# Optimization experiments

Hardware: AMD Instinct MI355X
Metric: run time of the kernel (lower is better)

## Reference

```python
import jax, jax.numpy as jnp
import numpy as np

D_MODEL = 2048
N_HEADS = 16
HEAD_DIM = D_MODEL // N_HEADS
BATCH = 2
SEQ = 2048


def rotate_half(x):
    x1, x2 = jnp.split(x, 2, axis=-1)
    return jnp.concatenate((-x2, x1), axis=-1)


def rope_emb(seq_len, head_dim, dtype=jnp.float32):
    inv_freq = 1.0 / (10000.0 ** (jnp.arange(0, head_dim, 2, dtype=jnp.float32) / head_dim))
    t = jnp.arange(seq_len, dtype=jnp.float32)
    freqs = jnp.einsum('i,j->ij', t, inv_freq)            # [S, D/2]
    emb = jnp.concatenate((freqs, freqs), axis=-1)        # [S, D]
    return emb[None, :, None, :].astype(dtype)            # [1, S, 1, D]


def apply_rope(x, emb):
    return x * jnp.cos(emb) + rotate_half(x) * jnp.sin(emb)


def setup_inputs() -> dict:
    key = jax.random.key(0)
    ks = jax.random.split(key, 5)
    s = 1.0 / np.sqrt(D_MODEL)
    return {
        'query': jax.random.normal(ks[0], (BATCH, SEQ, D_MODEL), jnp.float32),
        'Wq': jax.random.normal(ks[1], (D_MODEL, D_MODEL), jnp.float32) * s,
        'Wk': jax.random.normal(ks[2], (D_MODEL, D_MODEL), jnp.float32) * s,
        'Wv': jax.random.normal(ks[3], (D_MODEL, D_MODEL), jnp.float32) * s,
        'Wo': jax.random.normal(ks[4], (D_MODEL, D_MODEL), jnp.float32) * s,
    }


def reference(query, Wq, Wk, Wv, Wo):
    B, S, _ = query.shape
    # QKV projections (nn.Linear: x @ W.T), reshape to [B, S, H, Dh]
    q = (query @ Wq.T).reshape(B, S, N_HEADS, HEAD_DIM)
    k = (query @ Wk.T).reshape(B, S, N_HEADS, HEAD_DIM)
    v = (query @ Wv.T).reshape(B, S, N_HEADS, HEAD_DIM)
    emb = rope_emb(S, HEAD_DIM, q.dtype)
    q = apply_rope(q, emb)
    k = apply_rope(k, emb)
    # causal SDPA
    scale = HEAD_DIM ** -0.5
    scores = jnp.einsum('bqhd,bkhd->bhqk', q, k) * scale  # [B, H, S, S]
    causal = jnp.tril(jnp.ones((S, S), dtype=bool))
    scores = jnp.where(causal, scores, jnp.finfo(scores.dtype).min)
    attn = jax.nn.softmax(scores, axis=-1)
    out = jnp.einsum('bhqk,bkhd->bqhd', attn, v).reshape(B, S, D_MODEL)
    return out @ Wo.T
```

## Files before the change

kernel.cpp:

```cpp
#include <hip/hip_runtime.h>
#include <math.h>

#define BATCH 2
#define SEQ 2048
#define DMODEL 2048
#define NHEADS 16
#define HEADDIM 128
#define MTOT (BATCH * SEQ)
#define QKVLD 6144

typedef __attribute__((ext_vector_type(8))) _Float16 half8;
typedef __attribute__((ext_vector_type(4))) _Float16 half4;
typedef __attribute__((ext_vector_type(4))) float f32x4;

__device__ __forceinline__ void gl_lds16(const void* g, void* l) {
    __builtin_amdgcn_global_load_lds(
        (const __attribute__((address_space(1))) unsigned int*)g,
        (__attribute__((address_space(3))) unsigned int*)l, 16, 0, 0);
}

__global__ __launch_bounds__(256) void f2h_conv(const float* __restrict__ src,
                                                _Float16* __restrict__ dst) {
    size_t i = ((size_t)blockIdx.x * 256 + threadIdx.x) * 8;
    float4 a = *(const float4*)(src + i);
    float4 b = *(const float4*)(src + i + 4);
    union { uint4 u; _Float16 h[8]; } o;
    o.h[0] = (_Float16)a.x; o.h[1] = (_Float16)a.y;
    o.h[2] = (_Float16)a.z; o.h[3] = (_Float16)a.w;
    o.h[4] = (_Float16)b.x; o.h[5] = (_Float16)b.y;
    o.h[6] = (_Float16)b.z; o.h[7] = (_Float16)b.w;
    *(uint4*)(dst + i) = o.u;
}

__global__ __launch_bounds__(256) void f2h3_conv(const float* __restrict__ s0,
                                                 const float* __restrict__ s1,
                                                 const float* __restrict__ s2,
                                                 _Float16* __restrict__ dst) {
    const float* src = (blockIdx.y == 0) ? s0 : (blockIdx.y == 1) ? s1 : s2;
    size_t i = ((size_t)blockIdx.x * 256 + threadIdx.x) * 8;
    float4 a = *(const float4*)(src + i);
    float4 b = *(const float4*)(src + i + 4);
    union { uint4 u; _Float16 h[8]; } o;
    o.h[0] = (_Float16)a.x; o.h[1] = (_Float16)a.y;
    o.h[2] = (_Float16)a.z; o.h[3] = (_Float16)a.w;
    o.h[4] = (_Float16)b.x; o.h[5] = (_Float16)b.y;
    o.h[6] = (_Float16)b.z; o.h[7] = (_Float16)b.w;
    *(uint4*)(dst + (size_t)blockIdx.y * (DMODEL * DMODEL) + i) = o.u;
}

#define SB0  __builtin_amdgcn_sched_barrier(0)
#define BAR  __builtin_amdgcn_s_barrier()
#define VMW4 do { SB0; asm volatile("s_waitcnt vmcnt(4)"); SB0; } while (0)
#define VMW0 do { SB0; asm volatile("s_waitcnt vmcnt(0)"); SB0; } while (0)

template <bool F16OUT>
__global__ __launch_bounds__(512, 2) void gemm8p(const _Float16* __restrict__ A,
                                                 const _Float16* __restrict__ W,
                                                 void* __restrict__ Cout,
                                                 int M, int N, int K) {
    __shared__ __align__(16) _Float16 LAb[2][2][128][64];
    __shared__ __align__(16) _Float16 LBb[2][2][128][64];

    const int tid = threadIdx.x;
    const int lane = tid & 63;
    const int wave = tid >> 6;
    const int quad = lane >> 4;
    const int lcol = lane & 15;
    const int wr = wave >> 2;
    const int wc = wave & 3;
    const int m0 = blockIdx.y * 256;
    const int n0 = blockIdx.x * 256;

    const int srow = tid >> 3;
    const int sc8p = tid & 7;
    const int sc8l = sc8p ^ (srow & 7);

#define STA(BUF, HALF, KT)                                                     \
    do {                                                                       \
        _Pragma("unroll") for (int j = 0; j < 2; j++)                          \
            gl_lds16(A + (size_t)(m0 + (HALF)*128 + j*64 + srow) * K +         \
                         (KT)*64 + sc8l*8,                                     \
                     &LAb[BUF][HALF][j*64 + srow][sc8p*8]);                    \
    } while (0)
#define STB(BUF, HALF, KT)                                                     \
    do {                                                                       \
        _Pragma("unroll") for (int j = 0; j < 2; j++)                          \
            gl_lds16(W + (size_t)(n0 + (HALF)*128 + j*64 + srow) * K +         \
                         (KT)*64 + sc8l*8,                                     \
                     &LBb[BUF][HALF][j*64 + srow][sc8p*8]);                    \
    } while (0)

    auto rdA = [&](int buf, int mf, int ks) -> half8 {
        int R = mf * 16 + lcol;
        return *(const half8*)&LAb[buf][wr][R]
                [(ks * 32 + quad * 8) ^ ((lcol & 7) << 3)];
    };
    auto rdB = [&](int buf, int nf, int ks) -> half8 {
        int R = (wc & 1) * 64 + nf * 16 + lcol;
        return *(const half8*)&LBb[buf][wc >> 1][R]
                [(ks * 32 + quad * 8) ^ ((lcol & 7) << 3)];
    };

    f32x4 acc[8][4];
#pragma unroll
    for (int i = 0; i < 8; i++)
#pragma unroll
        for (int j = 0; j < 4; j++) acc[i][j] = (f32x4){0.f, 0.f, 0.f, 0.f};

#define KTILE4(BUF, S1, S2, S3, S4, W4)                                        \
    {                                                                          \
        half8 a[4][2], b[4][2];                                                \
                         \
        _Pragma("unroll") for (int mf = 0; mf < 4; mf++)                       \
            _Pragma("unroll") for (int ks = 0; ks < 2; ks++)                   \
                a[mf][ks] = rdA(BUF, mf, ks);                                  \
        _Pragma("unroll") for (int nf = 0; nf < 2; nf++)                       \
            _Pragma("unroll") for (int ks = 0; ks < 2; ks++)                   \
                b[nf][ks] = rdB(BUF, nf, ks);                                  \
        S1; SB0; BAR; SB0;                                                     \
        __builtin_amdgcn_s_setprio(1);                                         \
        _Pragma("unroll") for (int ks = 0; ks < 2; ks++)                       \
            _Pragma("unroll") for (int mf = 0; mf < 4; mf++)                   \
                _Pragma("unroll") for (int nf = 0; nf < 2; nf++)               \
                    acc[mf][nf] = __builtin_amdgcn_mfma_f32_16x16x32_f16(      \
                        a[mf][ks], b[nf][ks], acc[mf][nf], 0, 0, 0);           \
        __builtin_amdgcn_s_setprio(0); SB0; BAR; SB0;                          \
                                             \
        _Pragma("unroll") for (int nf = 0; nf < 2; nf++)                       \
            _Pragma("unroll") for (int ks = 0; ks < 2; ks++)                   \
                b[2 + nf][ks] = rdB(BUF, 2 + nf, ks);                          \
        S2; SB0; BAR; SB0;                                                     \
        __builtin_amdgcn_s_setprio(1);                                         \
        _Pragma("unroll") for (int ks = 0; ks < 2; ks++)                       \
            _Pragma("unroll") for (int mf = 0; mf < 4; mf++)                   \
                _Pragma("unroll") for (int nf = 0; nf < 2; nf++)               \
                    acc[mf][2 + nf] = __builtin_amdgcn_mfma_f32_16x16x32_f16(  \
                        a[mf][ks], b[2 + nf][ks], acc[mf][2 + nf], 0, 0, 0);   \
        __builtin_amdgcn_s_setprio(0); SB0; BAR; SB0;                          \
               \
        _Pragma("unroll") for (int mf = 0; mf < 4; mf++)                       \
            _Pragma("unroll") for (int ks = 0; ks < 2; ks++)                   \
                a[mf][ks] = rdA(BUF, 4 + mf, ks);                              \
        S3; SB0; BAR; SB0;                                                     \
        __builtin_amdgcn_s_setprio(1);                                         \
        _Pragma("unroll") for (int ks = 0; ks < 2; ks++)                       \
            _Pragma("unroll") for (int mf = 0; mf < 4; mf++)                   \
                _Pragma("unroll") for (int nf = 0; nf < 2; nf++)               \
                    acc[4 + mf][nf] = __builtin_amdgcn_mfma_f32_16x16x32_f16(  \
                        a[mf][ks], b[nf][ks], acc[4 + mf][nf], 0, 0, 0);       \
        __builtin_amdgcn_s_setprio(0); SB0; BAR; SB0;                          \
              \
        S4; W4; BAR; SB0;                                                      \
        __builtin_amdgcn_s_setprio(1);                                         \
        _Pragma("unroll") for (int ks = 0; ks < 2; ks++)                       \
            _Pragma("unroll") for (int mf = 0; mf < 4; mf++)                   \
                _Pragma("unroll") for (int nf = 0; nf < 2; nf++)               \
                    acc[4 + mf][2 + nf] =                                      \
                        __builtin_amdgcn_mfma_f32_16x16x32_f16(                \
                            a[mf][ks], b[2 + nf][ks], acc[4 + mf][2 + nf],     \
                            0, 0, 0);                                          \
        __builtin_amdgcn_s_setprio(0); SB0; BAR; SB0;                          \
    }

    STB(0, 0, 0); STB(0, 1, 0); STA(0, 0, 0); STA(0, 1, 0);
    STB(1, 0, 1); STB(1, 1, 1);
    VMW4; BAR; SB0;

    const int niter = K >> 7;
    for (int i = 0; i < niter - 1; ++i) {
        const int t0 = 2 * i;
        KTILE4(0, STA(1, 0, t0 + 1), STA(1, 1, t0 + 1),
                  STB(0, 0, t0 + 2), STB(0, 1, t0 + 2), VMW4);
        KTILE4(1, STA(0, 0, t0 + 2), STA(0, 1, t0 + 2),
                  STB(1, 0, t0 + 3), STB(1, 1, t0 + 3), VMW4);
    }
    {
        const int t0 = 2 * (niter - 1);
        KTILE4(0, STA(1, 0, t0 + 1), STA(1, 1, t0 + 1),
                  (void)0, (void)0, VMW0);
        KTILE4(1, (void)0, (void)0, (void)0, (void)0, (void)0);
    }

    float* Cf = (float*)Cout;
    _Float16* Ch = (_Float16*)Cout;
#pragma unroll
    for (int mf = 0; mf < 8; mf++)
#pragma unroll
        for (int nf = 0; nf < 4; nf++)
#pragma unroll
            for (int r = 0; r < 4; r++) {
                size_t row = m0 + wr * 128 + mf * 16 + quad * 4 + r;
                size_t col = n0 + wc * 64 + nf * 16 + lcol;
                if (F16OUT)
                    Ch[row * N + col] = (_Float16)acc[mf][nf][r];
                else
                    Cf[row * N + col] = acc[mf][nf][r];
            }
#undef KTILE4
#undef STA
#undef STB
}

__global__ __launch_bounds__(256) void rope_qk(_Float16* __restrict__ buf) {
    size_t idx = (size_t)blockIdx.x * 256 + threadIdx.x;
    int d = (int)(idx & 63);
    int h = (int)((idx >> 6) & (NHEADS - 1));
    int qk = (int)((idx >> 10) & 1);
    int m = (int)(idx >> 11);
    int s = m & (SEQ - 1);
    float scale = qk ? 1.0f : 0.08838834764831845f;
    float inv = __expf(-(float)d * 0.14391156831212787f);
    float f = (float)s * inv;
    float sn, cs;
    __sincosf(f, &sn, &cs);
    size_t base = (size_t)m * QKVLD + qk * DMODEL + h * HEADDIM + d;
    float x1 = (float)buf[base];
    float x2 = (float)buf[base + 64];
    buf[base]      = (_Float16)((x1 * cs - x2 * sn) * scale);
    buf[base + 64] = (_Float16)((x2 * cs + x1 * sn) * scale);
}

__global__ __launch_bounds__(256) void conv_v_t(const _Float16* __restrict__ src,
                                                _Float16* __restrict__ dst) {
    __shared__ __align__(16) _Float16 T[32][72];
    const int tid = threadIdx.x;
    const int s0 = blockIdx.x * 64;
    const int d0 = blockIdx.y * 32;
    const int bh = blockIdx.z;
    const int b = bh >> 4;
    const int h = bh & 15;

    {
        int s = tid >> 2;
        int d8 = (tid & 3) * 8;
        union { uint4 u; _Float16 hh[8]; } v;
        v.u = *(const uint4*)(src + (size_t)(b * SEQ + s0 + s) * QKVLD +
                              2 * DMODEL + h * HEADDIM + d0 + d8);
#pragma unroll
        for (int j = 0; j < 8; j++) T[d8 + j][s] = v.hh[j];
    }
    __syncthreads();

    int row = tid >> 3;
    int chunk = tid & 7;
    uint4 val = *(const uint4*)&T[row][chunk * 8];
    *(uint4*)(dst + ((size_t)(bh * HEADDIM + d0 + row)) * SEQ + s0 + chunk * 8) = val;
}

__global__ __launch_bounds__(512) void attn_mfma(const _Float16* __restrict__ qkv,
                                                 const _Float16* __restrict__ vtb,
                                                 _Float16* __restrict__ ab) {
    __shared__ __align__(16) _Float16 Ks[64][136];
    __shared__ __align__(16) _Float16 Vts[128][72];
    __shared__ __align__(16) _Float16 Ps[8][16][72];

    const int tid = threadIdx.x;
    const int wave = tid >> 6;
    const int lane = tid & 63;
    const int quad = lane >> 4;
    const int lcol = lane & 15;

    const int h = blockIdx.y;
    const int b = blockIdx.z;
    const int qtA = blockIdx.x;

    const int kr0 = tid >> 4;
    const int ko0 = (tid & 15) * 8;
    const int vr0 = tid >> 3;
    const int vo0 = (tid & 7) * 8;

    const _Float16* kbp = qkv + (size_t)b * SEQ * QKVLD + DMODEL + h * HEADDIM;
    const _Float16* vbp = vtb + ((size_t)(b * NHEADS + h) * HEADDIM) * SEQ;

    uint4 kA, kB, vA, vB;
#define ISSUE_LOAD(kb)                                                        \
    do {                                                                      \
        int _kb = (kb);                                                       \
        kA = *(const uint4*)(kbp + (size_t)(_kb + kr0) * QKVLD + ko0);        \
        kB = *(const uint4*)(kbp + (size_t)(_kb + 32 + kr0) * QKVLD + ko0);   \
        vA = *(const uint4*)(vbp + (size_t)vr0 * SEQ + _kb + vo0);            \
        vB = *(const uint4*)(vbp + (size_t)(vr0 + 64) * SEQ + _kb + vo0);     \
    } while (0)

    ISSUE_LOAD(0);

    for (int ph = 0; ph < 2; ++ph) {
        const int qt = ph ? (15 - qtA) : qtA;
        const int q0 = qt * 128 + wave * 16;
        const int nkt = 2 * qt + 2;

        half8 aq[4];
        {
            const _Float16* qrow =
                qkv + (size_t)(b * SEQ + q0 + lcol) * QKVLD + h * HEADDIM;
#pragma unroll
            for (int st = 0; st < 4; st++)
                aq[st] = *(const half8*)(qrow + quad * 8 + 32 * st);
        }

        f32x4 Of[8];
#pragma unroll
        for (int dt = 0; dt < 8; dt++) Of[dt] = (f32x4){0.f, 0.f, 0.f, 0.f};
        float m_s = -1e30f, l_s = 0.f;

        for (int kt = 0; kt < nkt; ++kt) {
            const int kbase = kt << 6;

            __syncthreads();
            *(uint4*)&Ks[kr0][ko0]        = kA;
            *(uint4*)&Ks[kr0 + 32][ko0]   = kB;
            *(uint4*)&Vts[vr0][vo0]       = vA;
            *(uint4*)&Vts[vr0 + 64][vo0]  = vB;
            __syncthreads();

            if (kt + 1 < nkt)      ISSUE_LOAD((kt + 1) << 6);
            else if (ph == 0)      ISSUE_LOAD(0);

            if (kbase > q0 + 15) continue;

            f32x4 Sc[4];
#pragma unroll
            for (int s = 0; s < 4; s++) {
                Sc[s] = (f32x4){0.f, 0.f, 0.f, 0.f};
#pragma unroll
                for (int st = 0; st < 4; st++) {
                    half8 bk = *(const half8*)&Ks[16 * s + lcol][quad * 8 + 32 * st];
                    Sc[s] = __builtin_amdgcn_mfma_f32_16x16x32_f16(bk, aq[st], Sc[s],
                                                                   0, 0, 0);
                }
            }

            if (kbase + 63 > q0) {
#pragma unroll
                for (int s = 0; s < 4; s++)
#pragma unroll
                    for (int r = 0; r < 4; r++)
                        if (kbase + 16 * s + quad * 4 + r > q0 + lcol)
                            Sc[s][r] = -1e30f;
            }

            float pmax = Sc[0][0];
#pragma unroll
            for (int s = 0; s < 4; s++)
#pragma unroll
                for (int r = 0; r < 4; r++) pmax = fmaxf(pmax, Sc[s][r]);
            pmax = fmaxf(pmax, __shfl_xor(pmax, 16));
            pmax = fmaxf(pmax, __shfl_xor(pmax, 32));

            if (!__all(pmax <= m_s + 5.0f)) {
                float mnew = fmaxf(m_s, pmax);
                float alpha = __expf(m_s - mnew);
                m_s = mnew;
                l_s *= alpha;
                float a0 = __shfl(alpha, quad * 4 + 0);
                float a1 = __shfl(alpha, quad * 4 + 1);
                float a2 = __shfl(alpha, quad * 4 + 2);
                float a3 = __shfl(alpha, quad * 4 + 3);
#pragma unroll
                for (int dt = 0; dt < 8; dt++) {
                    Of[dt][0] *= a0;
                    Of[dt][1] *= a1;
                    Of[dt][2] *= a2;
                    Of[dt][3] *= a3;
                }
            }

            float sum = 0.f;
#pragma unroll
            for (int s = 0; s < 4; s++)
#pragma unroll
                for (int r = 0; r < 4; r++) {
                    float p = __expf(Sc[s][r] - m_s);
                    Sc[s][r] = p;
                    sum += p;
                }
            sum += __shfl_xor(sum, 16);
            sum += __shfl_xor(sum, 32);
            l_s += sum;

#pragma unroll
            for (int s = 0; s < 4; s++) {
                union { half4 v; unsigned long long u; } pk;
                pk.v[0] = (_Float16)Sc[s][0];
                pk.v[1] = (_Float16)Sc[s][1];
                pk.v[2] = (_Float16)Sc[s][2];
                pk.v[3] = (_Float16)Sc[s][3];
                *(half4*)&Ps[wave][lcol][16 * s + 4 * quad] = pk.v;
            }

            half8 ap[2];
#pragma unroll
            for (int st = 0; st < 2; st++)
                ap[st] = *(const half8*)&Ps[wave][lcol][quad * 8 + 32 * st];
#pragma unroll
            for (int dt = 0; dt < 8; dt++) {
#pragma unroll
                for (int st = 0; st < 2; st++) {
                    half8 bv = *(const half8*)&Vts[16 * dt + lcol][quad * 8 + 32 * st];
                    Of[dt] = __builtin_amdgcn_mfma_f32_16x16x32_f16(ap[st], bv, Of[dt],
                                                                    0, 0, 0);
                }
            }
        }

        float invl = 1.f / l_s;
        float i0 = __shfl(invl, quad * 4 + 0);
        float i1 = __shfl(invl, quad * 4 + 1);
        float i2 = __shfl(invl, quad * 4 + 2);
        float i3 = __shfl(invl, quad * 4 + 3);
        _Float16* obase =
            ab + (size_t)(b * SEQ + q0 + quad * 4) * DMODEL + h * HEADDIM;
#pragma unroll
        for (int dt = 0; dt < 8; dt++) {
            obase[(size_t)0 * DMODEL + 16 * dt + lcol] = (_Float16)(Of[dt][0] * i0);
            obase[(size_t)1 * DMODEL + 16 * dt + lcol] = (_Float16)(Of[dt][1] * i1);
            obase[(size_t)2 * DMODEL + 16 * dt + lcol] = (_Float16)(Of[dt][2] * i2);
            obase[(size_t)3 * DMODEL + 16 * dt + lcol] = (_Float16)(Of[dt][3] * i3);
        }
    }
#undef ISSUE_LOAD
}

extern "C" void kernel_launch(void* const* d_in, const int* in_sizes, int n_in,
                              void* d_out, int out_size, void* d_ws, size_t ws_size,
                              hipStream_t stream) {
    const float* query = (const float*)d_in[0];
    const float* Wq = (const float*)d_in[1];
    const float* Wk = (const float*)d_in[2];
    const float* Wv = (const float*)d_in[3];
    const float* Wo = (const float*)d_in[4];
    float* out = (float*)d_out;

    const size_t MB = 1024 * 1024;
    char* w = (char*)d_ws;
    _Float16* xh   = (_Float16*)(w + 0 * MB);
    _Float16* ab   = (_Float16*)(w + 0 * MB);
    _Float16* qkvh = (_Float16*)(w + 16 * MB);
    _Float16* Wh3  = (_Float16*)(w + 64 * MB);
    _Float16* vtb  = (_Float16*)(w + 88 * MB);

    const int convX = (MTOT * DMODEL) / (256 * 8);
    const int convW = (DMODEL * DMODEL) / (256 * 8);
    const int ropeBlocks = (MTOT * 2 * NHEADS * 64) / 256;

    f2h_conv<<<convX, 256, 0, stream>>>(query, xh);
    f2h3_conv<<<dim3(convW, 3), 256, 0, stream>>>(Wq, Wk, Wv, Wh3);

    gemm8p<true><<<dim3(QKVLD / 256, MTOT / 256), 512, 0, stream>>>(
        xh, Wh3, qkvh, MTOT, QKVLD, DMODEL);

    rope_qk<<<ropeBlocks, 256, 0, stream>>>(qkvh);
    conv_v_t<<<dim3(SEQ / 64, HEADDIM / 32, BATCH * NHEADS), 256, 0, stream>>>(qkvh, vtb);

    attn_mfma<<<dim3(8, NHEADS, BATCH), 512, 0, stream>>>(qkvh, vtb, ab);

    f2h_conv<<<convW, 256, 0, stream>>>(Wo, Wh3);
    gemm8p<false><<<dim3(DMODEL / 256, MTOT / 256), 512, 0, stream>>>(
        ab, Wh3, out, MTOT, DMODEL, DMODEL);
}
```

Before: 439.4 us.

## Restructure causal attention to process two query tiles concurrently; add simpler output GEMM

The attention kernel no longer runs two sequential phases per block (tile qtA then 15-qtA). Instead, waves 0-3 take one query tile and waves 4-7 take the mirrored tile, and each wave handles 32 query rows as two 16-row sub-blocks that share K/V tiles from LDS. This is meant to halve the number of K/V loads and barriers per block and to increase MFMA work per LDS read, at the cost of more registers and more waves idling on short-tile iterations. The output projection also switches from the 256x256 8-wave pipelined GEMM to a simple 128x128 4-wave GEMM. That gives a grid of 512 blocks instead of 128, which should fill the CUs better, but it gives up the software pipelining.

```diff
diff --git a/kernel.cpp b/kernel.cpp
--- a/kernel.cpp
+++ b/kernel.cpp
@@ -110,7 +110,6 @@
 #define KTILE4(BUF, S1, S2, S3, S4, W4)                                        \
     {                                                                          \
         half8 a[4][2], b[4][2];                                                \
-                         \
         _Pragma("unroll") for (int mf = 0; mf < 4; mf++)                       \
             _Pragma("unroll") for (int ks = 0; ks < 2; ks++)                   \
                 a[mf][ks] = rdA(BUF, mf, ks);                                  \
@@ -125,7 +124,6 @@
                     acc[mf][nf] = __builtin_amdgcn_mfma_f32_16x16x32_f16(      \
                         a[mf][ks], b[nf][ks], acc[mf][nf], 0, 0, 0);           \
         __builtin_amdgcn_s_setprio(0); SB0; BAR; SB0;                          \
-                                             \
         _Pragma("unroll") for (int nf = 0; nf < 2; nf++)                       \
             _Pragma("unroll") for (int ks = 0; ks < 2; ks++)                   \
                 b[2 + nf][ks] = rdB(BUF, 2 + nf, ks);                          \
@@ -137,7 +135,6 @@
                     acc[mf][2 + nf] = __builtin_amdgcn_mfma_f32_16x16x32_f16(  \
                         a[mf][ks], b[2 + nf][ks], acc[mf][2 + nf], 0, 0, 0);   \
         __builtin_amdgcn_s_setprio(0); SB0; BAR; SB0;                          \
-               \
         _Pragma("unroll") for (int mf = 0; mf < 4; mf++)                       \
             _Pragma("unroll") for (int ks = 0; ks < 2; ks++)                   \
                 a[mf][ks] = rdA(BUF, 4 + mf, ks);                              \
@@ -149,7 +146,6 @@
                     acc[4 + mf][nf] = __builtin_amdgcn_mfma_f32_16x16x32_f16(  \
                         a[mf][ks], b[nf][ks], acc[4 + mf][nf], 0, 0, 0);       \
         __builtin_amdgcn_s_setprio(0); SB0; BAR; SB0;                          \
-              \
         S4; W4; BAR; SB0;                                                      \
         __builtin_amdgcn_s_setprio(1);                                         \
         _Pragma("unroll") for (int ks = 0; ks < 2; ks++)                       \
@@ -199,6 +195,75 @@
 #undef KTILE4
 #undef STA
 #undef STB
+}
+
+template <bool F16OUT>
+__global__ __launch_bounds__(256) void gemm_h(const _Float16* __restrict__ A,
+                                              const _Float16* __restrict__ W,
+                                              void* __restrict__ Cout,
+                                              int M, int N, int K) {
+    __shared__ __align__(16) _Float16 As[128 * 32];
+    __shared__ __align__(16) _Float16 Bs[128 * 32];
+
+    const int tid = threadIdx.x;
+    const int wv = tid >> 6;
+    const int ln = tid & 63;
+    const int quad = ln >> 4;
+    const int lcol = ln & 15;
+    const int m0 = blockIdx.y * 128;
+    const int n0 = blockIdx.x * 128;
+    const int wm = (wv >> 1) * 64;
+    const int wn = (wv & 1) * 64;
+
+    const int srow = ln >> 2;
+    const int kblk = (ln & 3) * 8;
+
+    f32x4 acc[4][4];
+#pragma unroll
+    for (int i = 0; i < 4; i++)
+#pragma unroll
+        for (int j = 0; j < 4; j++) acc[i][j] = (f32x4){0.f, 0.f, 0.f, 0.f};
+
+    for (int k0 = 0; k0 < K; k0 += 32) {
+        __syncthreads();
+#pragma unroll
+        for (int j = 0; j < 2; j++) {
+            int r = wv * 32 + j * 16 + srow;
+            gl_lds16(A + (size_t)(m0 + r) * K + k0 + kblk, &As[r * 32 + kblk]);
+            gl_lds16(W + (size_t)(n0 + r) * K + k0 + kblk, &Bs[r * 32 + kblk]);
+        }
+        __syncthreads();
+
+        half8 af[4], bf[4];
+#pragma unroll
+        for (int ms = 0; ms < 4; ms++)
+            af[ms] = *(const half8*)&As[(wm + ms * 16 + lcol) * 32 + quad * 8];
+#pragma unroll
+        for (int ns = 0; ns < 4; ns++)
+            bf[ns] = *(const half8*)&Bs[(wn + ns * 16 + lcol) * 32 + quad * 8];
+#pragma unroll
+        for (int ms = 0; ms < 4; ms++)
+#pragma unroll
+            for (int ns = 0; ns < 4; ns++)
+                acc[ms][ns] = __builtin_amdgcn_mfma_f32_16x16x32_f16(
+                    af[ms], bf[ns], acc[ms][ns], 0, 0, 0);
+    }
+
+    float* Cf = (float*)Cout;
+    _Float16* Ch = (_Float16*)Cout;
+#pragma unroll
+    for (int ms = 0; ms < 4; ms++)
+#pragma unroll
+        for (int ns = 0; ns < 4; ns++)
+#pragma unroll
+            for (int r = 0; r < 4; r++) {
+                size_t row = m0 + wm + ms * 16 + quad * 4 + r;
+                size_t col = n0 + wn + ns * 16 + lcol;
+                if (F16OUT)
+                    Ch[row * N + col] = (_Float16)acc[ms][ns][r];
+                else
+                    Cf[row * N + col] = acc[ms][ns][r];
+            }
 }
 
 __global__ __launch_bounds__(256) void rope_qk(_Float16* __restrict__ buf) {
@@ -264,6 +329,10 @@
     const int b = blockIdx.z;
     const int qtA = blockIdx.x;
 
+    const int wtile = (wave < 4) ? qtA : (15 - qtA);
+    const int q0w = wtile * 128 + (wave & 3) * 32;
+    const int nkt = 2 * (15 - qtA) + 2;
+
     const int kr0 = tid >> 4;
     const int ko0 = (tid & 15) * 8;
     const int vr0 = tid >> 3;
@@ -284,138 +353,201 @@
 
     ISSUE_LOAD(0);
 
-    for (int ph = 0; ph < 2; ++ph) {
-        const int qt = ph ? (15 - qtA) : qtA;
-        const int q0 = qt * 128 + wave * 16;
-        const int nkt = 2 * qt + 2;
-
-        half8 aq[4];
+    half8 aq0[4], aq1[4];
+    {
+        const _Float16* q0p = qkv + (size_t)(b * SEQ + q0w + lcol) * QKVLD + h * HEADDIM;
+        const _Float16* q1p = q0p + (size_t)16 * QKVLD;
+#pragma unroll
+        for (int st = 0; st < 4; st++) {
+            aq0[st] = *(const half8*)(q0p + quad * 8 + 32 * st);
+            aq1[st] = *(const half8*)(q1p + quad * 8 + 32 * st);
+        }
+    }
+
+    f32x4 Of0[8], Of1[8];
+#pragma unroll
+    for (int dt = 0; dt < 8; dt++) {
+        Of0[dt] = (f32x4){0.f, 0.f, 0.f, 0.f};
+        Of1[dt] = (f32x4){0.f, 0.f, 0.f, 0.f};
+    }
+    float m_s0 = -1e30f, l_s0 = 0.f;
+    float m_s1 = -1e30f, l_s1 = 0.f;
+
+    for (int kt = 0; kt < nkt; ++kt) {
+        const int kbase = kt << 6;
+
+        __syncthreads();
+        *(uint4*)&Ks[kr0][ko0]        = kA;
+        *(uint4*)&Ks[kr0 + 32][ko0]   = kB;
+        *(uint4*)&Vts[vr0][vo0]       = vA;
+        *(uint4*)&Vts[vr0 + 64][vo0]  = vB;
+        __syncthreads();
+
+        if (kt + 1 < nkt) ISSUE_LOAD((kt + 1) << 6);
+
+        if (kbase > q0w + 31) continue;
+
+        f32x4 Sc0[4], Sc1[4];
+#pragma unroll
+        for (int s = 0; s < 4; s++) {
+            Sc0[s] = (f32x4){0.f, 0.f, 0.f, 0.f};
+            Sc1[s] = (f32x4){0.f, 0.f, 0.f, 0.f};
+#pragma unroll
+            for (int st = 0; st < 4; st++) {
+                half8 bk = *(const half8*)&Ks[16 * s + lcol][quad * 8 + 32 * st];
+                Sc0[s] = __builtin_amdgcn_mfma_f32_16x16x32_f16(bk, aq0[st], Sc0[s], 0, 0, 0);
+                Sc1[s] = __builtin_amdgcn_mfma_f32_16x16x32_f16(bk, aq1[st], Sc1[s], 0, 0, 0);
+            }
+        }
+
+        if (kbase + 63 > q0w) {
+#pragma unroll
+            for (int s = 0; s < 4; s++)
+#pragma unroll
+                for (int r = 0; r < 4; r++) {
+                    int kk = kbase + 16 * s + quad * 4 + r;
+                    if (kk > q0w + lcol)      Sc0[s][r] = -1e30f;
+                    if (kk > q0w + 16 + lcol) Sc1[s][r] = -1e30f;
+                }
+        }
+
+        half8 ap0[2], ap1[2];
+
         {
-            const _Float16* qrow =
-                qkv + (size_t)(b * SEQ + q0 + lcol) * QKVLD + h * HEADDIM;
-#pragma unroll
-            for (int st = 0; st < 4; st++)
-                aq[st] = *(const half8*)(qrow + quad * 8 + 32 * st);
-        }
-
-        f32x4 Of[8];
-#pragma unroll
-        for (int dt = 0; dt < 8; dt++) Of[dt] = (f32x4){0.f, 0.f, 0.f, 0.f};
-        float m_s = -1e30f, l_s = 0.f;
-
-        for (int kt = 0; kt < nkt; ++kt) {
-            const int kbase = kt << 6;
-
-            __syncthreads();
-            *(uint4*)&Ks[kr0][ko0]        = kA;
-            *(uint4*)&Ks[kr0 + 32][ko0]   = kB;
-            *(uint4*)&Vts[vr0][vo0]       = vA;
-            *(uint4*)&Vts[vr0 + 64][vo0]  = vB;
-            __syncthreads();
-
-            if (kt + 1 < nkt)      ISSUE_LOAD((kt + 1) << 6);
-            else if (ph == 0)      ISSUE_LOAD(0);
-
-            if (kbase > q0 + 15) continue;
-
-            f32x4 Sc[4];
-#pragma unroll
-            for (int s = 0; s < 4; s++) {
-                Sc[s] = (f32x4){0.f, 0.f, 0.f, 0.f};
-#pragma unroll
-                for (int st = 0; st < 4; st++) {
-                    half8 bk = *(const half8*)&Ks[16 * s + lcol][quad * 8 + 32 * st];
-                    Sc[s] = __builtin_amdgcn_mfma_f32_16x16x32_f16(bk, aq[st], Sc[s],
-                                                                   0, 0, 0);
-                }
-            }
-
-            if (kbase + 63 > q0) {
-#pragma unroll
-                for (int s = 0; s < 4; s++)
-#pragma unroll
-                    for (int r = 0; r < 4; r++)
-                        if (kbase + 16 * s + quad * 4 + r > q0 + lcol)
-                            Sc[s][r] = -1e30f;
-            }
-
-            float pmax = Sc[0][0];
+            float pmax = Sc0[0][0];
 #pragma unroll
             for (int s = 0; s < 4; s++)
 #pragma unroll
-                for (int r = 0; r < 4; r++) pmax = fmaxf(pmax, Sc[s][r]);
+                for (int r = 0; r < 4; r++) pmax = fmaxf(pmax, Sc0[s][r]);
             pmax = fmaxf(pmax, __shfl_xor(pmax, 16));
             pmax = fmaxf(pmax, __shfl_xor(pmax, 32));
-
-            if (!__all(pmax <= m_s + 5.0f)) {
-                float mnew = fmaxf(m_s, pmax);
-                float alpha = __expf(m_s - mnew);
-                m_s = mnew;
-                l_s *= alpha;
+            if (!__all(pmax <= m_s0 + 5.0f)) {
+                float mnew = fmaxf(m_s0, pmax);
+                float alpha = __expf(m_s0 - mnew);
+                m_s0 = mnew;
+                l_s0 *= alpha;
                 float a0 = __shfl(alpha, quad * 4 + 0);
                 float a1 = __shfl(alpha, quad * 4 + 1);
                 float a2 = __shfl(alpha, quad * 4 + 2);
                 float a3 = __shfl(alpha, quad * 4 + 3);
 #pragma unroll
                 for (int dt = 0; dt < 8; dt++) {
-                    Of[dt][0] *= a0;
-                    Of[dt][1] *= a1;
-                    Of[dt][2] *= a2;
-                    Of[dt][3] *= a3;
+                    Of0[dt][0] *= a0; Of0[dt][1] *= a1;
+                    Of0[dt][2] *= a2; Of0[dt][3] *= a3;
                 }
             }
-
             float sum = 0.f;
 #pragma unroll
             for (int s = 0; s < 4; s++)
 #pragma unroll
                 for (int r = 0; r < 4; r++) {
-                    float p = __expf(Sc[s][r] - m_s);
-                    Sc[s][r] = p;
+                    float p = __expf(Sc0[s][r] - m_s0);
+                    Sc0[s][r] = p;
                     sum += p;
                 }
             sum += __shfl_xor(sum, 16);
             sum += __shfl_xor(sum, 32);
-            l_s += sum;
-
+            l_s0 += sum;
 #pragma unroll
             for (int s = 0; s < 4; s++) {
-                union { half4 v; unsigned long long u; } pk;
-                pk.v[0] = (_Float16)Sc[s][0];
-                pk.v[1] = (_Float16)Sc[s][1];
-                pk.v[2] = (_Float16)Sc[s][2];
-                pk.v[3] = (_Float16)Sc[s][3];
-                *(half4*)&Ps[wave][lcol][16 * s + 4 * quad] = pk.v;
-            }
-
-            half8 ap[2];
-#pragma unroll
-            for (int st = 0; st < 2; st++)
-                ap[st] = *(const half8*)&Ps[wave][lcol][quad * 8 + 32 * st];
-#pragma unroll
-            for (int dt = 0; dt < 8; dt++) {
-#pragma unroll
-                for (int st = 0; st < 2; st++) {
-                    half8 bv = *(const half8*)&Vts[16 * dt + lcol][quad * 8 + 32 * st];
-                    Of[dt] = __builtin_amdgcn_mfma_f32_16x16x32_f16(ap[st], bv, Of[dt],
-                                                                    0, 0, 0);
+                half4 pk;
+                pk[0] = (_Float16)Sc0[s][0]; pk[1] = (_Float16)Sc0[s][1];
+                pk[2] = (_Float16)Sc0[s][2]; pk[3] = (_Float16)Sc0[s][3];
+                *(half4*)&Ps[wave][lcol][16 * s + 4 * quad] = pk;
+            }
+            ap0[0] = *(const half8*)&Ps[wave][lcol][quad * 8];
+            ap0[1] = *(const half8*)&Ps[wave][lcol][quad * 8 + 32];
+        }
+
+        {
+            float pmax = Sc1[0][0];
+#pragma unroll
+            for (int s = 0; s < 4; s++)
+#pragma unroll
+                for (int r = 0; r < 4; r++) pmax = fmaxf(pmax, Sc1[s][r]);
+            pmax = fmaxf(pmax, __shfl_xor(pmax, 16));
+            pmax = fmaxf(pmax, __shfl_xor(pmax, 32));
+            if (!__all(pmax <= m_s1 + 5.0f)) {
+                float mnew = fmaxf(m_s1, pmax);
+                float alpha = __expf(m_s1 - mnew);
+                m_s1 = mnew;
+                l_s1 *= alpha;
+                float a0 = __shfl(alpha, quad * 4 + 0);
+                float a1 = __shfl(alpha, quad * 4 + 1);
+                float a2 = __shfl(alpha, quad * 4 + 2);
+                float a3 = __shfl(alpha, quad * 4 + 3);
+#pragma unroll
+                for (int dt = 0; dt < 8; dt++) {
+                    Of1[dt][0] *= a0; Of1[dt][1] *= a1;
+                    Of1[dt][2] *= a2; Of1[dt][3] *= a3;
                 }
             }
-        }
-
-        float invl = 1.f / l_s;
+            float sum = 0.f;
+#pragma unroll
+            for (int s = 0; s < 4; s++)
+#pragma unroll
+                for (int r = 0; r < 4; r++) {
+                    float p = __expf(Sc1[s][r] - m_s1);
+                    Sc1[s][r] = p;
+                    sum += p;
+                }
+            sum += __shfl_xor(sum, 16);
+            sum += __shfl_xor(sum, 32);
+            l_s1 += sum;
+#pragma unroll
+            for (int s = 0; s < 4; s++) {
+                half4 pk;
+                pk[0] = (_Float16)Sc1[s][0]; pk[1] = (_Float16)Sc1[s][1];
+                pk[2] = (_Float16)Sc1[s][2]; pk[3] = (_Float16)Sc1[s][3];
+                *(half4*)&Ps[wave][lcol][16 * s + 4 * quad] = pk;
+            }
+            ap1[0] = *(const half8*)&Ps[wave][lcol][quad * 8];
+            ap1[1] = *(const half8*)&Ps[wave][lcol][quad * 8 + 32];
+        }
+
+#pragma unroll
+        for (int dt = 0; dt < 8; dt++) {
+#pragma unroll
+            for (int st = 0; st < 2; st++) {
+                half8 bv = *(const half8*)&Vts[16 * dt + lcol][quad * 8 + 32 * st];
+                Of0[dt] = __builtin_amdgcn_mfma_f32_16x16x32_f16(
+                    st == 0 ? ap0[0] : ap0[1], bv, Of0[dt], 0, 0, 0);
+                Of1[dt] = __builtin_amdgcn_mfma_f32_16x16x32_f16(
+                    st == 0 ? ap1[0] : ap1[1], bv, Of1[dt], 0, 0, 0);
+            }
+        }
+    }
+
+    {
+        float invl = 1.f / l_s0;
         float i0 = __shfl(invl, quad * 4 + 0);
         float i1 = __shfl(invl, quad * 4 + 1);
         float i2 = __shfl(invl, quad * 4 + 2);
         float i3 = __shfl(invl, quad * 4 + 3);
         _Float16* obase =
-            ab + (size_t)(b * SEQ + q0 + quad * 4) * DMODEL + h * HEADDIM;
+            ab + (size_t)(b * SEQ + q0w + quad * 4) * DMODEL + h * HEADDIM;
 #pragma unroll
         for (int dt = 0; dt < 8; dt++) {
-            obase[(size_t)0 * DMODEL + 16 * dt + lcol] = (_Float16)(Of[dt][0] * i0);
-            obase[(size_t)1 * DMODEL + 16 * dt + lcol] = (_Float16)(Of[dt][1] * i1);
-            obase[(size_t)2 * DMODEL + 16 * dt + lcol] = (_Float16)(Of[dt][2] * i2);
-            obase[(size_t)3 * DMODEL + 16 * dt + lcol] = (_Float16)(Of[dt][3] * i3);
+            obase[(size_t)0 * DMODEL + 16 * dt + lcol] = (_Float16)(Of0[dt][0] * i0);
+            obase[(size_t)1 * DMODEL + 16 * dt + lcol] = (_Float16)(Of0[dt][1] * i1);
+            obase[(size_t)2 * DMODEL + 16 * dt + lcol] = (_Float16)(Of0[dt][2] * i2);
+            obase[(size_t)3 * DMODEL + 16 * dt + lcol] = (_Float16)(Of0[dt][3] * i3);
+        }
+    }
+    {
+        float invl = 1.f / l_s1;
+        float i0 = __shfl(invl, quad * 4 + 0);
+        float i1 = __shfl(invl, quad * 4 + 1);
+        float i2 = __shfl(invl, quad * 4 + 2);
+        float i3 = __shfl(invl, quad * 4 + 3);
+        _Float16* obase =
+            ab + (size_t)(b * SEQ + q0w + 16 + quad * 4) * DMODEL + h * HEADDIM;
+#pragma unroll
+        for (int dt = 0; dt < 8; dt++) {
+            obase[(size_t)0 * DMODEL + 16 * dt + lcol] = (_Float16)(Of1[dt][0] * i0);
+            obase[(size_t)1 * DMODEL + 16 * dt + lcol] = (_Float16)(Of1[dt][1] * i1);
+            obase[(size_t)2 * DMODEL + 16 * dt + lcol] = (_Float16)(Of1[dt][2] * i2);
+            obase[(size_t)3 * DMODEL + 16 * dt + lcol] = (_Float16)(Of1[dt][3] * i3);
         }
     }
 #undef ISSUE_LOAD
@@ -455,6 +587,6 @@
     attn_mfma<<<dim3(8, NHEADS, BATCH), 512, 0, stream>>>(qkvh, vtb, ab);
 
     f2h_conv<<<convW, 256, 0, stream>>>(Wo, Wh3);
-    gemm8p<false><<<dim3(DMODEL / 256, MTOT / 256), 512, 0, stream>>>(
+    gemm_h<false><<<dim3(DMODEL / 128, MTOT / 128), 256, 0, stream>>>(
         ab, Wh3, out, MTOT, DMODEL, DMODEL);
 }
```

Measured after the change: 415.2 us. 5.5% less time.
